# Performance work log

Hardware: AMD Instinct MI355X
Metric: run time of the kernel (lower is better)

Reference implementation:

```python
import jax, jax.numpy as jnp
import numpy as np

C = 192
NH = 8
DH = C // NH
WD, WH, WW = 6, 8, 8
SD, SH, SW = 3, 4, 4
B0, D, H, W = 1, 24, 64, 64  # divisible by window -> no padding
N = WD * WH * WW
EPS = 1e-5


def _layernorm(x, w, b):
    m = jnp.mean(x, axis=-1, keepdims=True)
    v = jnp.mean(jnp.square(x - m), axis=-1, keepdims=True)
    return (x - m) * jax.lax.rsqrt(v + EPS) * w + b


def _window_partition(x):
    # x: (B, Dp, Hp, Wp, C) -> (B*nW, N, C)
    B, Dp, Hp, Wp, Cc = x.shape
    x = x.reshape(B, Dp // WD, WD, Hp // WH, WH, Wp // WW, WW, Cc)
    x = x.transpose(0, 1, 3, 5, 2, 4, 6, 7)
    return x.reshape(-1, N, Cc)


def _window_reverse(win, B, Dp, Hp, Wp):
    Cc = win.shape[-1]
    x = win.reshape(B, Dp // WD, Hp // WH, Wp // WW, WD, WH, WW, Cc)
    x = x.transpose(0, 1, 4, 2, 5, 3, 6, 7)
    return x.reshape(B, Dp, Hp, Wp, Cc)


def _shift_attn_mask(Dp, Hp, Wp, dtype):
    # static numpy construction (Swin shifted-window mask)
    img = np.zeros((Dp, Hp, Wp), dtype=np.int32)
    cnt = 0
    d_sl = (slice(0, -WD), slice(-WD, -SD), slice(-SD, None))
    h_sl = (slice(0, -WH), slice(-WH, -SH), slice(-SH, None))
    w_sl = (slice(0, -WW), slice(-WW, -SW), slice(-SW, None))
    for ds in d_sl:
        for hs in h_sl:
            for ws in w_sl:
                img[ds, hs, ws] = cnt
                cnt += 1
    m = img.reshape(Dp // WD, WD, Hp // WH, WH, Wp // WW, WW)
    m = m.transpose(0, 2, 4, 1, 3, 5).reshape(-1, N)  # (nW, N)
    diff = m[:, None, :] - m[:, :, None]
    neg = np.finfo(np.float32).min
    mask = np.where(diff != 0, neg, 0.0).astype(np.float32)
    return jnp.asarray(mask, dtype=dtype)  # (nW, N, N)


def setup_inputs() -> dict:
    key = jax.random.key(0)
    ks = jax.random.split(key, 4)
    return {
        "q_map": jax.random.normal(ks[0], (B0, C, D, H, W), jnp.float32),
        "k_map": jax.random.normal(ks[1], (B0, C, D, H, W), jnp.float32),
        "v_map": jax.random.normal(ks[2], (B0, C, D, H, W), jnp.float32),
        "norm_q_w": jnp.ones((C,), jnp.float32),
        "norm_q_b": jnp.zeros((C,), jnp.float32),
        "norm_kv_w": jnp.ones((C,), jnp.float32),
        "norm_kv_b": jnp.zeros((C,), jnp.float32),
        "proj_w": jax.random.normal(ks[3], (C, C), jnp.float32) * 0.02,
        "proj_b": jnp.zeros((C,), jnp.float32),
    }


def reference(q_map, k_map, v_map, norm_q_w, norm_q_b, norm_kv_w, norm_kv_b, proj_w, proj_b):
    # (B,C,D,H,W) -> (B,D,H,W,C)
    q = q_map.transpose(0, 2, 3, 4, 1)
    k = k_map.transpose(0, 2, 3, 4, 1)
    v = v_map.transpose(0, 2, 3, 4, 1)
    # dims already divisible by window -> no pad
    Dp, Hp, Wp = D, H, W
    # cyclic shift
    q = jnp.roll(q, shift=(-SD, -SH, -SW), axis=(1, 2, 3))
    k = jnp.roll(k, shift=(-SD, -SH, -SW), axis=(1, 2, 3))
    v = jnp.roll(v, shift=(-SD, -SH, -SW), axis=(1, 2, 3))
    # window partition -> (Bwin, N, C)
    qw = _layernorm(_window_partition(q), norm_q_w, norm_q_b)
    kw = _layernorm(_window_partition(k), norm_kv_w, norm_kv_b)
    vw = _layernorm(_window_partition(v), norm_kv_w, norm_kv_b)
    Bwin = qw.shape[0]
    nW = Bwin // B0
    # heads
    qh = qw.reshape(Bwin, N, NH, DH).transpose(0, 2, 1, 3)
    kh = kw.reshape(Bwin, N, NH, DH).transpose(0, 2, 1, 3)
    vh = vw.reshape(Bwin, N, NH, DH).transpose(0, 2, 1, 3)
    scale = 1.0 / jnp.sqrt(jnp.asarray(DH, qh.dtype))
    scores = jnp.einsum('bhqd,bhkd->bhqk', qh, kh) * scale  # (Bwin,NH,N,N)
    mask = _shift_attn_mask(Dp, Hp, Wp, scores.dtype)  # (nW,N,N)
    scores = scores.reshape(B0, nW, NH, N, N) + mask[None, :, None]
    attn = jax.nn.softmax(scores, axis=-1).reshape(Bwin, NH, N, N)
    out = jnp.einsum('bhqk,bhkd->bhqd', attn, vh)
    out = out.transpose(0, 2, 1, 3).reshape(Bwin, N, C)
    out = jnp.einsum('bnc,oc->bno', out, proj_w) + proj_b
    out = _window_reverse(out, B0, Dp, Hp, Wp)
    out = jnp.roll(out, shift=(SD, SH, SW), axis=(1, 2, 3))
    return out.transpose(0, 4, 1, 2, 3)  # (B,C,D,H,W)
```

## Files before the change

kernel.cpp:

```cpp
#include <hip/hip_runtime.h>

typedef float f4v __attribute__((ext_vector_type(4)));
typedef _Float16 h8 __attribute__((ext_vector_type(8)));
typedef _Float16 h4 __attribute__((ext_vector_type(4)));
typedef _Float16 h2 __attribute__((ext_vector_type(2)));
typedef __fp16 f16x2 __attribute__((ext_vector_type(2)));


__device__ __forceinline__ float fast_exp2(float x) {
#if __has_builtin(__builtin_amdgcn_exp2f)
    return __builtin_amdgcn_exp2f(x);
#else
    return exp2f(x);
#endif
}
__device__ __forceinline__ float fast_rcp(float x) {
#if __has_builtin(__builtin_amdgcn_rcpf)
    return __builtin_amdgcn_rcpf(x);
#else
    return 1.0f / x;
#endif
}

__device__ __forceinline__ int region_slot(int n, int wi, int hi, int wj) {
    int s = 0;
    if (wi == 3 && (n >> 6) >= 3) s += 4;
    if (hi == 7 && ((n >> 3) & 7) >= 4) s += 2;
    if (wj == 7 && (n & 7) >= 4) s += 1;
    return s;
}

__global__ __launch_bounds__(256) void ln_stage_kernel(
    const float* __restrict__ q, const float* __restrict__ k, const float* __restrict__ v,
    const float* __restrict__ nqw, const float* __restrict__ nqb,
    const float* __restrict__ nkw, const float* __restrict__ nkb,
    _Float16* __restrict__ Qs, _Float16* __restrict__ Ks, _Float16* __restrict__ Vs)
{
    const int tid = threadIdx.x;
    const int bid = blockIdx.x;
    const int tensor = blockIdx.y;
    const int d = bid >> 5;
    const int h2 = bid & 31;

    const float* src = (tensor == 0) ? q : (tensor == 1) ? k : v;
    const float* gam = (tensor == 0) ? nqw : nkw;
    const float* bet = (tensor == 0) ? nqb : nkb;
    _Float16* dst = (tensor == 0) ? Qs : (tensor == 1) ? Ks : Vs;
    const float scale = (tensor == 0) ? (0.20412414523193154f * 1.44269504088896340f) : 1.0f;

    __shared__ __attribute__((aligned(16))) _Float16 tile[192][132];
    __shared__ __attribute__((aligned(16))) float psum4[4][128];
    __shared__ __attribute__((aligned(16))) float psq4[4][128];
    __shared__ float smean[128];
    __shared__ float srstd[128];
    __shared__ float sgam[192];
    __shared__ float sbet[192];

    if (tid < 192) { sgam[tid] = gam[tid]; sbet[tid] = bet[tid]; }

    const int lane = tid & 63;
    const int wid = tid >> 6;
    const int cg = tid >> 5;
    const int fp = tid & 31;

    {
        const float* base = src + (size_t)d * 4096 + (size_t)(h2 * 2) * 64 + fp * 4;
        f4v s4 = {}, ss4 = {};
        #pragma unroll
        for (int r = 0; r < 24; ++r) {
            const int c = r * 8 + cg;
            f4v x = *(const f4v*)(base + (size_t)c * 98304);
            s4 += x;
            ss4 += x * x;
            h4 hx;
            hx[0] = (_Float16)x[0]; hx[1] = (_Float16)x[1];
            hx[2] = (_Float16)x[2]; hx[3] = (_Float16)x[3];
            *(h4*)&tile[c][fp * 4] = hx;
        }
        #pragma unroll
        for (int m = 0; m < 4; ++m) {
            s4[m] += __shfl_xor(s4[m], 32);
            ss4[m] += __shfl_xor(ss4[m], 32);
        }
        if (lane < 32) {
            *(f4v*)&psum4[wid][lane * 4] = s4;
            *(f4v*)&psq4[wid][lane * 4] = ss4;
        }
    }
    __syncthreads();

    if (tid < 128) {
        float S = psum4[0][tid] + psum4[1][tid] + psum4[2][tid] + psum4[3][tid];
        float SS = psq4[0][tid] + psq4[1][tid] + psq4[2][tid] + psq4[3][tid];
        float mean = S * (1.0f / 192.0f);
        float var = SS * (1.0f / 192.0f) - mean * mean;
        smean[tid] = mean;
        srstd[tid] = rsqrtf(var + 1e-5f);
    }
    __syncthreads();

    {
        const int t = tid & 127;
        const int p = tid >> 7;
        const float mean = smean[t];
        const float rstd = srstd[t];
        const int h = h2 * 2 + (t >> 6);
        const int w = t & 63;
        int d_r = d + 21; if (d_r >= 24) d_r -= 24;
        int h_r = h + 60; if (h_r >= 64) h_r -= 64;
        int w_r = w + 60; if (w_r >= 64) w_r -= 64;
        const int wi = d_r / 6, td = d_r - wi * 6;
        const int hi = h_r >> 3, th = h_r & 7;
        const int wj = w_r >> 3, tw = w_r & 7;
        const int win = (wi * 8 + hi) * 8 + wj;
        const int n = (td * 8 + th) * 8 + tw;
        #pragma unroll
        for (int hh2 = 0; hh2 < 4; ++hh2) {
            const int head = p * 4 + hh2;
            _Float16* outp = dst + (size_t)(head * 256 + win) * 9216 + n * 24;
            #pragma unroll
            for (int cc = 0; cc < 3; ++cc) {
                const int c = head * 24 + cc * 8;
                h8 hv;
                #pragma unroll
                for (int j = 0; j < 8; ++j) {
                    float x = ((float)tile[c + j][t] - mean) * rstd * sgam[c + j] + sbet[c + j];
                    hv[j] = (_Float16)(x * scale);
                }
                *(h8*)(outp + cc * 8) = hv;
            }
        }
    }
}

__global__ __launch_bounds__(256) void wconv_kernel(const float* __restrict__ w,
                                                    _Float16* __restrict__ wb)
{
    int i = blockIdx.x * 256 + threadIdx.x;
    if (i < 192 * 192) wb[i] = (_Float16)w[i];
}

__device__ __forceinline__ void attn_epilogue(
    f4v o0, f4v o1, _Float16* __restrict__ Op,
    _Float16* __restrict__ AOw, int q0, int lane, int l15, int g)
{
    #pragma unroll
    for (int j = 0; j < 4; ++j) {
        float rs = __shfl(o1[j], (g << 4) | 8);
        float inv = fast_rcp(rs);
        const int r = 4 * g + j;
        Op[r * 24 + l15] = (_Float16)(o0[j] * inv);
        if (l15 < 8) Op[r * 24 + 16 + l15] = (_Float16)(o1[j] * inv);
    }
    asm volatile("s_waitcnt lgkmcnt(0)" ::: "memory");
    if (lane < 48) {
        h8 ov = *(const h8*)(Op + lane * 8);
        *(h8*)(AOw + (size_t)q0 * 24 + lane * 8) = ov;
    }
    asm volatile("" ::: "memory");
}

__global__ __launch_bounds__(512, 2) void attn_kernel(
    const _Float16* __restrict__ Qs, const _Float16* __restrict__ Ks,
    const _Float16* __restrict__ Vs, _Float16* __restrict__ AOs)
{
    const int win = blockIdx.x;
    const int head = blockIdx.y;
    const int tid = threadIdx.x;
    const int lane = tid & 63;
    const int wid = tid >> 6;
    const int l15 = lane & 15;
    const int g = lane >> 4;

    __shared__ __attribute__((aligned(16))) _Float16 Kh[384 * 36];
    __shared__ __attribute__((aligned(16))) _Float16 Vt[25 * 388];
    __shared__ __attribute__((aligned(16))) _Float16 Ob[8][2][16 * 24];

    const int wi = win >> 6, hi = (win >> 3) & 7, wj = win & 7;

    const size_t slab = (size_t)(head * 256 + win) * 9216;
    const _Float16* Kw = Ks + slab;
    const _Float16* Vw = Vs + slab;
    const _Float16* Qw = Qs + slab;
    _Float16* AOw = AOs + slab;

    const _Float16 mreg = (_Float16)6.32455532f;

    h8 qreg[3];
    #pragma unroll
    for (int qt = 0; qt < 3; ++qt) {
        h8 z = {};
        if (g < 3) {
            z = *(const h8*)(Qw + (size_t)(wid * 48 + qt * 16 + l15) * 24 + g * 8);
        } else {
            int slot = region_slot(wid * 48 + qt * 16 + l15, wi, hi, wj);
            #pragma unroll
            for (int j = 0; j < 8; ++j) z[j] = (slot == j) ? mreg : (_Float16)0.f;
        }
        qreg[qt] = z;
    }

    {
        const h8* K8 = (const h8*)Kw;
        const h8* V8 = (const h8*)Vw;
        #pragma unroll
        for (int it = 0; it < 5; ++it) {
            int idx = it * 512 + tid;
            if (idx < 1152) {
                int n = idx / 3;
                int ch = idx - n * 3;
                *(h8*)(Kh + n * 36 + ch * 8) = K8[idx];
            } else if (idx < 2304) {
                int i = idx - 1152;
                int n = i / 3;
                int ch = i - n * 3;
                h8 vv = V8[i];
                #pragma unroll
                for (int j = 0; j < 8; ++j) Vt[(ch * 8 + j) * 388 + n] = vv[j];
            }
        }
        if (tid < 384) {
            int slot = region_slot(tid, wi, hi, wj);
            h8 t;
            #pragma unroll
            for (int j = 0; j < 8; ++j) t[j] = (slot == j) ? mreg : (_Float16)0.f;
            *(h8*)(Kh + tid * 36 + 24) = t;
            Vt[24 * 388 + tid] = (_Float16)1.f;
        }
    }
    __syncthreads();

    const int v1row = (l15 < 8) ? (16 + l15) : 24;
    const int q0w = wid * 48;

    f4v o0_0 = {}, o1_0 = {}, o0_1 = {}, o1_1 = {};
    #pragma unroll
    for (int mt = 0; mt < 24; ++mt) {
        h8 kf = *(const h8*)(Kh + (16 * mt + l15) * 36 + g * 8);
        h4 v0 = *(const h4*)(Vt + l15 * 388 + 16 * mt + 4 * g);
        h4 v1 = *(const h4*)(Vt + v1row * 388 + 16 * mt + 4 * g);
        const f4v cinit = {-46.f, -46.f, -46.f, -46.f};

        {
            f4v s4 = __builtin_amdgcn_mfma_f32_16x16x32_f16(kf, qreg[0], cinit, 0, 0, 0);
            float p0 = fast_exp2(s4[0]), p1 = fast_exp2(s4[1]);
            float p2 = fast_exp2(s4[2]), p3 = fast_exp2(s4[3]);
            union { f16x2 gp[2]; h4 v; } pu;
            pu.gp[0] = __builtin_amdgcn_cvt_pkrtz(p0, p1);
            pu.gp[1] = __builtin_amdgcn_cvt_pkrtz(p2, p3);
            o0_0 = __builtin_amdgcn_mfma_f32_16x16x16f16(pu.v, v0, o0_0, 0, 0, 0);
            o1_0 = __builtin_amdgcn_mfma_f32_16x16x16f16(pu.v, v1, o1_0, 0, 0, 0);
        }
        {
            f4v s4 = __builtin_amdgcn_mfma_f32_16x16x32_f16(kf, qreg[1], cinit, 0, 0, 0);
            float p0 = fast_exp2(s4[0]), p1 = fast_exp2(s4[1]);
            float p2 = fast_exp2(s4[2]), p3 = fast_exp2(s4[3]);
            union { f16x2 gp[2]; h4 v; } pu;
            pu.gp[0] = __builtin_amdgcn_cvt_pkrtz(p0, p1);
            pu.gp[1] = __builtin_amdgcn_cvt_pkrtz(p2, p3);
            o0_1 = __builtin_amdgcn_mfma_f32_16x16x16f16(pu.v, v0, o0_1, 0, 0, 0);
            o1_1 = __builtin_amdgcn_mfma_f32_16x16x16f16(pu.v, v1, o1_1, 0, 0, 0);
        }
    }

    attn_epilogue(o0_0, o1_0, Ob[wid][0], AOw, q0w,      lane, l15, g);
    attn_epilogue(o0_1, o1_1, Ob[wid][1], AOw, q0w + 16, lane, l15, g);

    f4v o0a = {}, o0b = {}, o1a = {}, o1b = {};
    #pragma unroll
    for (int mt = 0; mt < 24; ++mt) {
        h8 kf = *(const h8*)(Kh + (16 * mt + l15) * 36 + g * 8);
        h4 v0 = *(const h4*)(Vt + l15 * 388 + 16 * mt + 4 * g);
        h4 v1 = *(const h4*)(Vt + v1row * 388 + 16 * mt + 4 * g);
        const f4v cinit = {-46.f, -46.f, -46.f, -46.f};
        f4v s4 = __builtin_amdgcn_mfma_f32_16x16x32_f16(kf, qreg[2], cinit, 0, 0, 0);
        float p0 = fast_exp2(s4[0]), p1 = fast_exp2(s4[1]);
        float p2 = fast_exp2(s4[2]), p3 = fast_exp2(s4[3]);
        union { f16x2 gp[2]; h4 v; } pu;
        pu.gp[0] = __builtin_amdgcn_cvt_pkrtz(p0, p1);
        pu.gp[1] = __builtin_amdgcn_cvt_pkrtz(p2, p3);
        if (mt & 1) {
            o0b = __builtin_amdgcn_mfma_f32_16x16x16f16(pu.v, v0, o0b, 0, 0, 0);
            o1b = __builtin_amdgcn_mfma_f32_16x16x16f16(pu.v, v1, o1b, 0, 0, 0);
        } else {
            o0a = __builtin_amdgcn_mfma_f32_16x16x16f16(pu.v, v0, o0a, 0, 0, 0);
            o1a = __builtin_amdgcn_mfma_f32_16x16x16f16(pu.v, v1, o1a, 0, 0, 0);
        }
    }
    attn_epilogue(o0a + o0b, o1a + o1b, Ob[wid][0], AOw, q0w + 32, lane, l15, g);
}

__global__ __launch_bounds__(256) void proj_wb_kernel(
    const _Float16* __restrict__ AOs, const _Float16* __restrict__ Wb,
    const float* __restrict__ bias, float* __restrict__ out)
{
    const int bid = blockIdx.x;
    const int dd = bid >> 6;
    const int hh = bid & 63;
    const int tid = threadIdx.x;
    const int lane = tid & 63, wid = tid >> 6;
    const int l15 = lane & 15, g = lane >> 4;

    __shared__ __attribute__((aligned(16))) unsigned char lmem[192 * 68 * 4];
    _Float16* Arows = (_Float16*)lmem;
    float* tileT = (float*)lmem;

    int d_r = dd + 21; if (d_r >= 24) d_r -= 24;
    int h_r = hh + 60; if (h_r >= 64) h_r -= 64;
    const int wi = d_r / 6, td = d_r - wi * 6;
    const int hi = h_r >> 3, th = h_r & 7;
    const int winbase = (wi * 8 + hi) * 8;
    const int nbase = (td * 8 + th) * 8;

    #pragma unroll
    for (int it = 0; it < 6; ++it) {
        int idx = it * 256 + tid;
        int t = idx / 24;
        int ch = idx - t * 24;
        int w_r = t + 60; if (w_r >= 64) w_r -= 64;
        int win = winbase + (w_r >> 3);
        int n = nbase + (w_r & 7);
        int head = ch / 3, sub = ch - 3 * head;
        h8 v = *(const h8*)(AOs + (size_t)(head * 256 + win) * 9216
                                + (size_t)n * 24 + sub * 8);
        *(h8*)(Arows + t * 200 + ch * 8) = v;
    }
    __syncthreads();

    h8 af[6];
    #pragma unroll
    for (int kk = 0; kk < 6; ++kk)
        af[kk] = *(const h8*)(Arows + (wid * 16 + l15) * 200 + kk * 32 + g * 8);
    __syncthreads();

    f4v acc[12];
    #pragma unroll
    for (int n = 0; n < 12; ++n) {
        f4v a = {};
        #pragma unroll
        for (int kk = 0; kk < 6; ++kk) {
            h8 bf = *(const h8*)(Wb + (size_t)(n * 16 + l15) * 192 + kk * 32 + g * 8);
            a = __builtin_amdgcn_mfma_f32_16x16x32_f16(af[kk], bf, a, 0, 0, 0);
        }
        acc[n] = a;
    }

    #pragma unroll
    for (int n = 0; n < 12; ++n) {
        float b = bias[n * 16 + l15];
        f4v vv = acc[n];
        vv[0] += b; vv[1] += b; vv[2] += b; vv[3] += b;
        *(f4v*)(tileT + (n * 16 + l15) * 68 + wid * 16 + g * 4) = vv;
    }
    __syncthreads();

    float* obase = out + (size_t)dd * 4096 + hh * 64;
    #pragma unroll
    for (int r = 0; r < 3; ++r) {
        const int c = r * 64 + (tid >> 2);
        float* orow = obase + (size_t)c * 98304;
        const float* trow = tileT + c * 68;
        #pragma unroll
        for (int q = 0; q < 4; ++q) {
            const int w0 = q * 16 + (tid & 3) * 4;
            f4v v = *(const f4v*)(trow + w0);
            *(f4v*)(orow + w0) = v;
        }
    }
}

extern "C" void kernel_launch(void* const* d_in, const int* in_sizes, int n_in,
                              void* d_out, int out_size, void* d_ws, size_t ws_size,
                              hipStream_t stream) {
    const float* q_map = (const float*)d_in[0];
    const float* k_map = (const float*)d_in[1];
    const float* v_map = (const float*)d_in[2];
    const float* nqw = (const float*)d_in[3];
    const float* nqb = (const float*)d_in[4];
    const float* nkw = (const float*)d_in[5];
    const float* nkb = (const float*)d_in[6];
    const float* pw = (const float*)d_in[7];
    const float* pb = (const float*)d_in[8];
    float* out = (float*)d_out;

    _Float16* ws = (_Float16*)d_ws;
    const size_t BUF = (size_t)8 * 256 * 384 * 24;
    _Float16* Qs = ws;
    _Float16* Ks = ws + BUF;
    _Float16* Vs = ws + 2 * BUF;
    _Float16* AOs = ws + 3 * BUF;
    _Float16* Wb = ws + 4 * BUF;

    ln_stage_kernel<<<dim3(768, 3), 256, 0, stream>>>(q_map, k_map, v_map,
                                                      nqw, nqb, nkw, nkb, Qs, Ks, Vs);
    wconv_kernel<<<144, 256, 0, stream>>>(pw, Wb);
    attn_kernel<<<dim3(256, 8), 512, 0, stream>>>(Qs, Ks, Vs, AOs);
    proj_wb_kernel<<<1536, 256, 0, stream>>>(AOs, Wb, pb, out);
}
```

Baseline: 194.5 us.

## Make LayerNorm stage persistent with register prefetch of next row

The LayerNorm/partition kernel becomes a persistent grid of 512 blocks. Each block loops over 9 single-row tiles (64 positions × 192 channels) across q, k and v, instead of launching 2304 blocks that each handle two rows. The global loads for the next tile are issued into registers before the current tile is normalized and scattered. This overlaps load latency with compute, using a double-buffered shared tile and reloading gamma/beta when the tensor switches. In exchange it uses more registers (48 floats held across the loop) and has fewer blocks to hide latency.

```diff
diff --git a/kernel.cpp b/kernel.cpp
--- a/kernel.cpp
+++ b/kernel.cpp
@@ -38,96 +38,119 @@
 {
     const int tid = threadIdx.x;
     const int bid = blockIdx.x;
-    const int tensor = blockIdx.y;
-    const int d = bid >> 5;
-    const int h2 = bid & 31;
-
-    const float* src = (tensor == 0) ? q : (tensor == 1) ? k : v;
-    const float* gam = (tensor == 0) ? nqw : nkw;
-    const float* bet = (tensor == 0) ? nqb : nkb;
-    _Float16* dst = (tensor == 0) ? Qs : (tensor == 1) ? Ks : Vs;
-    const float scale = (tensor == 0) ? (0.20412414523193154f * 1.44269504088896340f) : 1.0f;
-
-    __shared__ __attribute__((aligned(16))) _Float16 tile[192][132];
-    __shared__ __attribute__((aligned(16))) float psum4[4][128];
-    __shared__ __attribute__((aligned(16))) float psq4[4][128];
-    __shared__ float smean[128];
-    __shared__ float srstd[128];
+
+    __shared__ __attribute__((aligned(16))) _Float16 tile[2][192][70];
+    __shared__ __attribute__((aligned(16))) float psum4[4][64];
+    __shared__ __attribute__((aligned(16))) float psq4[4][64];
+    __shared__ float smean[64];
+    __shared__ float srstd[64];
     __shared__ float sgam[192];
     __shared__ float sbet[192];
 
-    if (tid < 192) { sgam[tid] = gam[tid]; sbet[tid] = bet[tid]; }
-
     const int lane = tid & 63;
     const int wid = tid >> 6;
-    const int cg = tid >> 5;
-    const int fp = tid & 31;
-
+    const int c0 = tid >> 4;
+    const int col = (tid & 15) << 2;
+    const float qscale = 0.20412414523193154f * 1.44269504088896340f;
+
+    if (tid < 192) { sgam[tid] = nqw[tid]; sbet[tid] = nqb[tid]; }
+    f4v xr[12];
     {
-        const float* base = src + (size_t)d * 4096 + (size_t)(h2 * 2) * 64 + fp * 4;
-        f4v s4 = {}, ss4 = {};
+        const int d = bid >> 6, h = bid & 63;
+        const float* base = q + (size_t)d * 4096 + (size_t)h * 64 + col;
         #pragma unroll
-        for (int r = 0; r < 24; ++r) {
-            const int c = r * 8 + cg;
-            f4v x = *(const f4v*)(base + (size_t)c * 98304);
-            s4 += x;
-            ss4 += x * x;
-            h4 hx;
-            hx[0] = (_Float16)x[0]; hx[1] = (_Float16)x[1];
-            hx[2] = (_Float16)x[2]; hx[3] = (_Float16)x[3];
-            *(h4*)&tile[c][fp * 4] = hx;
-        }
-        #pragma unroll
-        for (int m = 0; m < 4; ++m) {
-            s4[m] += __shfl_xor(s4[m], 32);
-            ss4[m] += __shfl_xor(ss4[m], 32);
-        }
-        if (lane < 32) {
-            *(f4v*)&psum4[wid][lane * 4] = s4;
-            *(f4v*)&psq4[wid][lane * 4] = ss4;
-        }
-    }
-    __syncthreads();
-
-    if (tid < 128) {
-        float S = psum4[0][tid] + psum4[1][tid] + psum4[2][tid] + psum4[3][tid];
-        float SS = psq4[0][tid] + psq4[1][tid] + psq4[2][tid] + psq4[3][tid];
-        float mean = S * (1.0f / 192.0f);
-        float var = SS * (1.0f / 192.0f) - mean * mean;
-        smean[tid] = mean;
-        srstd[tid] = rsqrtf(var + 1e-5f);
-    }
-    __syncthreads();
-
-    {
-        const int t = tid & 127;
-        const int p = tid >> 7;
-        const float mean = smean[t];
-        const float rstd = srstd[t];
-        const int h = h2 * 2 + (t >> 6);
-        const int w = t & 63;
-        int d_r = d + 21; if (d_r >= 24) d_r -= 24;
-        int h_r = h + 60; if (h_r >= 64) h_r -= 64;
-        int w_r = w + 60; if (w_r >= 64) w_r -= 64;
-        const int wi = d_r / 6, td = d_r - wi * 6;
-        const int hi = h_r >> 3, th = h_r & 7;
-        const int wj = w_r >> 3, tw = w_r & 7;
-        const int win = (wi * 8 + hi) * 8 + wj;
-        const int n = (td * 8 + th) * 8 + tw;
-        #pragma unroll
-        for (int hh2 = 0; hh2 < 4; ++hh2) {
-            const int head = p * 4 + hh2;
-            _Float16* outp = dst + (size_t)(head * 256 + win) * 9216 + n * 24;
-            #pragma unroll
-            for (int cc = 0; cc < 3; ++cc) {
-                const int c = head * 24 + cc * 8;
-                h8 hv;
+        for (int r = 0; r < 12; ++r)
+            xr[r] = *(const f4v*)(base + (size_t)(r * 16 + c0) * 98304);
+    }
+
+    for (int i = 0; i < 9; ++i) {
+        const int gs = i * 512 + bid;
+        const int tensor = i / 3;
+        const int s = gs - tensor * 1536;
+        const int d = s >> 6, h = s & 63;
+        const int cur = i & 1;
+        _Float16* dst = (tensor == 0) ? Qs : (tensor == 1) ? Ks : Vs;
+        const float scale = (tensor == 0) ? qscale : 1.0f;
+
+        if (i == 3 || i == 6) {
+            __syncthreads();
+            if (tid < 192) { sgam[tid] = nkw[tid]; sbet[tid] = nkb[tid]; }
+        }
+
+        {
+            f4v s4 = {}, ss4 = {};
+            #pragma unroll
+            for (int r = 0; r < 12; ++r) {
+                f4v x = xr[r];
+                s4 += x;
+                ss4 += x * x;
+                h4 hx;
+                hx[0] = (_Float16)x[0]; hx[1] = (_Float16)x[1];
+                hx[2] = (_Float16)x[2]; hx[3] = (_Float16)x[3];
+                *(h4*)&tile[cur][r * 16 + c0][col] = hx;
+            }
+            #pragma unroll
+            for (int m = 0; m < 4; ++m) {
+                s4[m] += __shfl_xor(s4[m], 16);  s4[m] += __shfl_xor(s4[m], 32);
+                ss4[m] += __shfl_xor(ss4[m], 16); ss4[m] += __shfl_xor(ss4[m], 32);
+            }
+            if (lane < 16) {
+                *(f4v*)&psum4[wid][lane * 4] = s4;
+                *(f4v*)&psq4[wid][lane * 4] = ss4;
+            }
+        }
+        __syncthreads();
+
+        if (tid < 64) {
+            float S = psum4[0][tid] + psum4[1][tid] + psum4[2][tid] + psum4[3][tid];
+            float SS = psq4[0][tid] + psq4[1][tid] + psq4[2][tid] + psq4[3][tid];
+            float mean = S * (1.0f / 192.0f);
+            float var = SS * (1.0f / 192.0f) - mean * mean;
+            smean[tid] = mean;
+            srstd[tid] = rsqrtf(var + 1e-5f);
+        }
+
+        if (i < 8) {
+            const int gs2 = gs + 512;
+            const int t2 = (i + 1) / 3;
+            const int s2 = gs2 - t2 * 1536;
+            const int d2 = s2 >> 6, h2 = s2 & 63;
+            const float* src2 = (t2 == 0) ? q : (t2 == 1) ? k : v;
+            const float* base2 = src2 + (size_t)d2 * 4096 + (size_t)h2 * 64 + col;
+            #pragma unroll
+            for (int r = 0; r < 12; ++r)
+                xr[r] = *(const f4v*)(base2 + (size_t)(r * 16 + c0) * 98304);
+        }
+        __syncthreads();
+
+        {
+            const int wpos = tid >> 2;
+            const int p = tid & 3;
+            const float mean = smean[wpos];
+            const float rstd = srstd[wpos];
+            int d_r = d + 21; if (d_r >= 24) d_r -= 24;
+            int h_r = h + 60; if (h_r >= 64) h_r -= 64;
+            int w_r = wpos + 60; if (w_r >= 64) w_r -= 64;
+            const int wi = d_r / 6, td = d_r - wi * 6;
+            const int hi = h_r >> 3, th = h_r & 7;
+            const int wj = w_r >> 3, tw = w_r & 7;
+            const int win = (wi * 8 + hi) * 8 + wj;
+            const int n = (td * 8 + th) * 8 + tw;
+            #pragma unroll
+            for (int hh2 = 0; hh2 < 2; ++hh2) {
+                const int head = p * 2 + hh2;
+                _Float16* outp = dst + (size_t)(head * 256 + win) * 9216 + n * 24;
                 #pragma unroll
-                for (int j = 0; j < 8; ++j) {
-                    float x = ((float)tile[c + j][t] - mean) * rstd * sgam[c + j] + sbet[c + j];
-                    hv[j] = (_Float16)(x * scale);
+                for (int cc = 0; cc < 3; ++cc) {
+                    const int c = head * 24 + cc * 8;
+                    h8 hv;
+                    #pragma unroll
+                    for (int j = 0; j < 8; ++j) {
+                        float x = ((float)tile[cur][c + j][wpos] - mean) * rstd * sgam[c + j] + sbet[c + j];
+                        hv[j] = (_Float16)(x * scale);
+                    }
+                    *(h8*)(outp + cc * 8) = hv;
                 }
-                *(h8*)(outp + cc * 8) = hv;
             }
         }
     }
@@ -391,8 +414,8 @@
     _Float16* AOs = ws + 3 * BUF;
     _Float16* Wb = ws + 4 * BUF;
 
-    ln_stage_kernel<<<dim3(768, 3), 256, 0, stream>>>(q_map, k_map, v_map,
-                                                      nqw, nqb, nkw, nkb, Qs, Ks, Vs);
+    ln_stage_kernel<<<512, 256, 0, stream>>>(q_map, k_map, v_map,
+                                             nqw, nqb, nkw, nkb, Qs, Ks, Vs);
     wconv_kernel<<<144, 256, 0, stream>>>(pw, Wb);
     attn_kernel<<<dim3(256, 8), 512, 0, stream>>>(Qs, Ks, Vs, AOs);
     proj_wb_kernel<<<1536, 256, 0, stream>>>(AOs, Wb, pb, out);
```

Result: no change. 191.7 us (-1.4%).
